# Performance work log

Hardware: AMD Instinct MI355X
Metric: run time of the kernel (lower is better)

## Reference

```python
import jax, jax.numpy as jnp
import numpy as np

N = 20000   # nodes
E = 40000   # directed edges
F_IN = 13   # dataset.num_features
G = 1000    # graphs in batch
DIMS = [(13, 32), (32, 64), (64, 64)]  # (M_in, M_out) per NNConv layer


def setup_inputs() -> dict:
    key = jax.random.key(0)
    ks = list(jax.random.split(key, 32))
    inp = {}
    inp["x"] = jax.random.normal(ks[0], (N, F_IN), jnp.float32)
    inp["edge_index"] = jax.random.randint(ks[1], (2, E), 0, N, dtype=jnp.int32)
    inp["edge_attr"] = jax.random.uniform(ks[2], (E, 5), dtype=jnp.float32)
    inp["batch"] = jnp.sort(jax.random.randint(ks[3], (N,), 0, G, dtype=jnp.int32))
    i = 4
    for l, (mi, mo) in enumerate(DIMS):
        inp[f"w1_{l}"] = jax.random.normal(ks[i], (5, 128), jnp.float32) / np.sqrt(5.0).astype(np.float32); i += 1
        inp[f"b1_{l}"] = jnp.zeros((128,), jnp.float32)
        inp[f"w2_{l}"] = jax.random.normal(ks[i], (128, mi * mo), jnp.float32) / np.sqrt(128.0).astype(np.float32); i += 1
        inp[f"b2_{l}"] = jnp.zeros((mi * mo,), jnp.float32)
        inp[f"root_{l}"] = jax.random.normal(ks[i], (mi, mo), jnp.float32) / np.sqrt(float(mi)).astype(np.float32); i += 1
        inp[f"bias_{l}"] = jnp.zeros((mo,), jnp.float32)
    inp["fc1_w"] = jax.random.normal(ks[i], (64, 32), jnp.float32) / 8.0; i += 1
    inp["fc1_b"] = jnp.zeros((32,), jnp.float32)
    inp["fc2_w"] = jax.random.normal(ks[i], (32, 16), jnp.float32) / np.sqrt(32.0).astype(np.float32); i += 1
    inp["fc2_b"] = jnp.zeros((16,), jnp.float32)
    inp["fc3_w"] = jax.random.normal(ks[i], (16, 1), jnp.float32) / 4.0; i += 1
    inp["fc3_b"] = jnp.zeros((1,), jnp.float32)
    return inp


def _nnconv(x, src, dst, edge_attr, w1, b1, w2, b2, root, bias, mi, mo):
    # edge MLP: [E,5] -> [E,128] -> [E, mi*mo] per-edge weight matrices
    h = jax.nn.relu(edge_attr @ w1 + b1)
    We = (h @ w2 + b2).reshape(-1, mi, mo)          # [E, mi, mo]
    msg = jnp.einsum('ei,eio->eo', x[src], We)      # gather + per-edge matmul
    agg = jax.ops.segment_sum(msg, dst, num_segments=x.shape[0])  # scatter-add
    return x @ root + agg + bias                    # NNConv root weight + bias


def _forward(x, edge_index, edge_attr, batch, convs, fc1_w, fc1_b, fc2_w, fc2_b, fc3_w, fc3_b):
    src, dst = edge_index[0], edge_index[1]
    for (mi, mo), (w1, b1, w2, b2, root, bias) in zip(DIMS, convs):
        x = jax.nn.elu(_nnconv(x, src, dst, edge_attr, w1, b1, w2, b2, root, bias, mi, mo))
    # scatter_mean pooling over graphs
    sums = jax.ops.segment_sum(x, batch, num_segments=G)
    cnt = jax.ops.segment_sum(jnp.ones((x.shape[0],), x.dtype), batch, num_segments=G)
    xg = sums / jnp.maximum(cnt, 1.0)[:, None]
    xg = jax.nn.elu(xg @ fc1_w + fc1_b)
    xg = jax.nn.elu(xg @ fc2_w + fc2_b)
    return (xg @ fc3_w + fc3_b).reshape(-1)


def reference(x, edge_index, edge_attr, batch,
              w1_0, b1_0, w2_0, b2_0, root_0, bias_0,
              w1_1, b1_1, w2_1, b2_1, root_1, bias_1,
              w1_2, b1_2, w2_2, b2_2, root_2, bias_2,
              fc1_w, fc1_b, fc2_w, fc2_b, fc3_w, fc3_b):
    convs = [(w1_0, b1_0, w2_0, b2_0, root_0, bias_0),
             (w1_1, b1_1, w2_1, b2_1, root_1, bias_1),
             (w1_2, b1_2, w2_2, b2_2, root_2, bias_2)]
    return _forward(x, edge_index, edge_attr, batch, convs,
                    fc1_w, fc1_b, fc2_w, fc2_b, fc3_w, fc3_b)
```

## Files before the change

### kernel.cpp

```cpp
#include <hip/hip_runtime.h>
#include <stdint.h>
#include <math.h>

typedef _Float16 half8_t __attribute__((ext_vector_type(8)));
typedef float floatx4 __attribute__((ext_vector_type(4)));

#define NN 20000
#define NE 40000
#define NG 1000
#define NBLK 313
#define NSPLIT 4

__global__ __launch_bounds__(256) void prep_fused_kernel(
    const float* __restrict__ x, _Float16* __restrict__ e16,
    const float* __restrict__ w2a, const float* __restrict__ b2a, _Float16* __restrict__ oa,
    const float* __restrict__ w2b, const float* __restrict__ b2b, _Float16* __restrict__ ob,
    const float* __restrict__ w2c, const float* __restrict__ b2c, _Float16* __restrict__ oc,
    int* __restrict__ deg)
{
  if (blockIdx.x < 1250) {
    int idx = blockIdx.x * 256 + threadIdx.x;
    int n = idx >> 4, i = idx & 15;
    e16[idx] = (i < 13) ? (_Float16)x[(size_t)n * 13 + i] : (_Float16)0.f;
    return;
  }
  if (blockIdx.x >= 1680) {
    int n = (blockIdx.x - 1680) * 256 + threadIdx.x;
    if (n < NN) deg[n] = 0;
    return;
  }
  const int TOT0 = 68 * 2 * 64, TOT1 = 132 * 4 * 64, TOT2 = 264 * 4 * 64;
  int idx = (blockIdx.x - 1250) * 256 + threadIdx.x;
  const float *w2, *b2; _Float16* op; int mi, mo, mpsh, CT;
  if (idx < TOT0) { w2 = w2a; b2 = b2a; op = oa; mi = 13; mo = 32; mpsh = 4; CT = 2; }
  else if (idx < TOT0 + TOT1) { idx -= TOT0; w2 = w2b; b2 = b2b; op = ob; mi = 32; mo = 64; mpsh = 5; CT = 4; }
  else if (idx < TOT0 + TOT1 + TOT2) { idx -= TOT0 + TOT1; w2 = w2c; b2 = b2c; op = oc; mi = 64; mo = 64; mpsh = 6; CT = 4; }
  else return;
  int l = idx & 63;
  int ct = (idx >> 6) % CT;
  int c = idx / (64 * CT);
  int q = l >> 4;
  int n = ct * 16 + (l & 15);
  int mask = (1 << mpsh) - 1;
  half8_t v;
#pragma unroll
  for (int j = 0; j < 8; ++j) {
    int r = c * 32 + q * 8 + j;
    int k = r >> mpsh, i = r & mask;
    float f = 0.f;
    if (i < mi) {
      if (k < 128) f = w2[(size_t)(k * mi + i) * mo + n];
      else if (k == 128) f = b2[(size_t)i * mo + n];
    }
    v[j] = (_Float16)f;
  }
  *(half8_t*)(op + (size_t)idx * 8) = v;
}

__global__ __launch_bounds__(256) void deg_kernel(const int* __restrict__ dst, int* __restrict__ deg) {
  int e = blockIdx.x * 256 + threadIdx.x;
  if (e < NE) atomicAdd(&deg[dst[e]], 1);
}

__global__ __launch_bounds__(1024) void scan_kernel(
    const int* __restrict__ deg, int* __restrict__ row_ptr, int* __restrict__ cursor)
{
  constexpr int CH = 20;
  __shared__ int wsum[16];
  int t = threadIdx.x;
  int lane = t & 63, w = t >> 6;
  int base = t * CH;
  int local[CH];
#pragma unroll
  for (int i = 0; i < CH; ++i) {
    int n = base + i;
    local[i] = (n < NN) ? deg[n] : 0;
  }
  int s = 0;
#pragma unroll
  for (int i = 0; i < CH; ++i) s += local[i];
  int sc = s;
#pragma unroll
  for (int d = 1; d < 64; d <<= 1) {
    int v = __shfl_up(sc, d, 64);
    if (lane >= d) sc += v;
  }
  if (lane == 63) wsum[w] = sc;
  __syncthreads();
  if (w == 0 && lane < 16) {
    int v = wsum[lane];
    int scc = v;
#pragma unroll
    for (int d = 1; d < 16; d <<= 1) {
      int u = __shfl_up(scc, d, 64);
      if (lane >= d) scc += u;
    }
    wsum[lane] = scc - v;
  }
  __syncthreads();
  int run = wsum[w] + (sc - s);
#pragma unroll
  for (int i = 0; i < CH; ++i) {
    int n = base + i;
    if (n < NN) { row_ptr[n] = run; cursor[n] = run; run += local[i]; }
    else if (n == NN) row_ptr[NN] = run;
  }
}

__global__ __launch_bounds__(256) void fill_kernel(
    const int* __restrict__ dst, int* __restrict__ cursor, int* __restrict__ eids)
{
  int e = blockIdx.x * 256 + threadIdx.x;
  if (e < NE) { int p = atomicAdd(&cursor[dst[e]], 1); eids[p] = e; }
}

template <int MIP, int MO, int NCC, int KCNT>
__global__ __launch_bounds__(256, 4) void msg9_kernel(
    const float* __restrict__ ea, const float* __restrict__ w1,
    const float* __restrict__ b1, const _Float16* __restrict__ xe,
    const int* __restrict__ src,
    const _Float16* __restrict__ w2h, _Float16* __restrict__ msgp)
{
  constexpr int EPB = 128;
  constexpr int CT = MO / 16;
  constexpr int CHB = CT * 1024;
  constexpr int XV = (MIP == 64) ? 2 : 1;
  constexpr int KH = (KCNT + 1) >> 1;

  __shared__ uint4 wsb[2][CHB / 16];
  __shared__ _Float16 h16[KCNT * EPB];
  __shared__ float w1s[5 * 128 + 128];

  const int t = threadIdx.x;
  const int wave = t >> 6, lane = t & 63;
  const int l15 = lane & 15, q = lane >> 4;
  const int split = blockIdx.x / NBLK;
  const int e0 = (blockIdx.x % NBLK) * EPB;
  const int c0 = NCC * split;
  const int kg0 = KCNT * split;

  const char* wgp = (const char*)w2h + (size_t)c0 * CHB;
  uint4 ra4, rb4; uint2 ra2, rb2;
  if constexpr (CT == 4) {
    ra4 = *(const uint4*)(wgp + t * 16);
    rb4 = *(const uint4*)(wgp + CHB + t * 16);
  } else {
    ra2 = *(const uint2*)(wgp + t * 8);
    rb2 = *(const uint2*)(wgp + CHB + t * 8);
  }

  const int wbase = wave * 32;
  half8_t xf[2][XV];
#pragma unroll
  for (int s = 0; s < 2; ++s) {
    int eg = e0 + wbase + s * 16 + l15; if (eg >= NE) eg = NE - 1;
    const _Float16* xr = xe + (size_t)src[eg] * MIP;
    int i0 = (MIP == 16) ? (q & 1) * 8 : q * 8;
    xf[s][0] = *(const half8_t*)(xr + i0);
    if constexpr (MIP == 64)
      xf[s][XV - 1] = *(const half8_t*)(xr + 32 + q * 8);
  }

  const int te = t & 127;
  float ear[5];
  {
    int eg = e0 + te; if (eg >= NE) eg = NE - 1;
#pragma unroll
    for (int j = 0; j < 5; ++j) ear[j] = ea[(size_t)eg * 5 + j];
  }
  for (int i = t; i < 768; i += 256) w1s[i] = (i < 640) ? w1[i] : b1[i - 640];
  __syncthreads();

  {
    int kh = t >> 7;
    int klo = kh * KH;
    int khi = klo + KH; if (khi > KCNT) khi = KCNT;
    for (int kl = klo; kl < khi; ++kl) {
      int kg = kg0 + kl;
      float v;
      if (kg < 128) {
        v = w1s[640 + kg];
#pragma unroll
        for (int j = 0; j < 5; ++j) v = fmaf(ear[j], w1s[j * 128 + kg], v);
        v = fmaxf(v, 0.f);
      } else v = (kg == 128) ? 1.f : 0.f;
      h16[kl * EPB + te] = (_Float16)v;
    }
  }
  __syncthreads();

  floatx4 acc[2][CT];
#pragma unroll
  for (int s = 0; s < 2; ++s)
#pragma unroll
    for (int b = 0; b < CT; ++b) acc[s][b] = (floatx4){0.f, 0.f, 0.f, 0.f};

#pragma unroll 2
  for (int cc = 0; cc < NCC; ++cc) {
    const bool odd = (cc & 1) != 0;
    if constexpr (CT == 4) wsb[cc & 1][t] = odd ? rb4 : ra4;
    else ((uint2*)wsb[cc & 1])[t] = odd ? rb2 : ra2;
    if (cc + 2 < NCC) {
      const char* np = wgp + (size_t)(cc + 2) * CHB;
      if constexpr (CT == 4) {
        if (odd) rb4 = *(const uint4*)(np + t * 16); else ra4 = *(const uint4*)(np + t * 16);
      } else {
        if (odd) rb2 = *(const uint2*)(np + t * 8); else ra2 = *(const uint2*)(np + t * 8);
      }
    }
    __syncthreads();
    const _Float16* wb = (const _Float16*)wsb[cc & 1];
    half8_t bf[CT];
#pragma unroll
    for (int b = 0; b < CT; ++b)
      bf[b] = *(const half8_t*)(wb + (b * 64 + lane) * 8);
    int kl;
    if constexpr (MIP == 64) kl = cc >> 1;
    else if constexpr (MIP == 32) kl = cc;
    else kl = 2 * cc + (q >> 1);
#pragma unroll
    for (int s = 0; s < 2; ++s) {
      _Float16 hv = h16[kl * EPB + wbase + s * 16 + l15];
      half8_t af;
      if constexpr (MIP == 64) af = xf[s][cc & 1] * hv;
      else af = xf[s][0] * hv;
#pragma unroll
      for (int b = 0; b < CT; ++b)
        acc[s][b] = __builtin_amdgcn_mfma_f32_16x16x32_f16(af, bf[b], acc[s][b], 0, 0, 0);
    }
  }

  _Float16* mp = msgp + (size_t)split * NE * MO;
#pragma unroll
  for (int s = 0; s < 2; ++s) {
    int rowb = wbase + s * 16 + q * 4;
#pragma unroll
    for (int b = 0; b < CT; ++b) {
      int n = b * 16 + l15;
#pragma unroll
      for (int r = 0; r < 4; ++r) {
        int row = rowb + r;
        int e = e0 + row;
        if (e < NE) mp[(size_t)e * MO + n] = (_Float16)acc[s][b][r];
      }
    }
  }
}

template <int MIN_, int XST, int MO, int FINAL>
__global__ __launch_bounds__(256) void gather_kernel(
    const _Float16* __restrict__ e16in, const float* __restrict__ root,
    const float* __restrict__ bias, const int* __restrict__ row_ptr,
    const int* __restrict__ eids, const _Float16* __restrict__ msgp,
    _Float16* __restrict__ oute, float* __restrict__ outf)
{
  constexpr int NPB = 256 / MO;
  int n = blockIdx.x * NPB + threadIdx.x / MO;
  int o = threadIdx.x % MO;
  if (n >= NN) return;
  float a = bias[o];
#pragma unroll
  for (int i = 0; i < MIN_; ++i)
    a = fmaf((float)e16in[(size_t)n * XST + i], root[i * MO + o], a);
  int r0 = row_ptr[n], r1 = row_ptr[n + 1];
  for (int j = r0; j < r1; ++j) {
    int e = eids[j];
#pragma unroll
    for (int s = 0; s < NSPLIT; ++s)
      a += (float)msgp[((size_t)s * NE + e) * MO + o];
  }
  if constexpr (FINAL) {
    outf[(size_t)n * MO + o] = a;
  } else {
    float v = a > 0.f ? a : (expf(a) - 1.f);
    oute[(size_t)n * MO + o] = (_Float16)v;
  }
}

__global__ __launch_bounds__(64) void pool_fc_kernel(
    const float* __restrict__ xn2, const int* __restrict__ batch,
    const float* __restrict__ f1w, const float* __restrict__ f1b,
    const float* __restrict__ f2w, const float* __restrict__ f2b,
    const float* __restrict__ f3w, const float* __restrict__ f3b,
    float* __restrict__ out)
{
  __shared__ float xg[64]; __shared__ float a1[32]; __shared__ float a2[16];
  int g = blockIdx.x, t = threadIdx.x;
  int lo = 0, hi = NN;
  while (lo < hi) { int m = (lo + hi) >> 1; if (batch[m] < g) lo = m + 1; else hi = m; }
  int start = lo; hi = NN;
  while (lo < hi) { int m = (lo + hi) >> 1; if (batch[m] <= g) lo = m + 1; else hi = m; }
  int end = lo;
  float acc = 0.f;
  for (int n = start; n < end; ++n) {
    float v = xn2[(size_t)n * 64 + t];
    acc += v > 0.f ? v : (expf(v) - 1.f);
  }
  float c = (end > start) ? (float)(end - start) : 1.f;
  xg[t] = acc / c;
  __syncthreads();
  if (t < 32) {
    float a = f1b[t];
    for (int i = 0; i < 64; ++i) a = fmaf(xg[i], f1w[i * 32 + t], a);
    a1[t] = a > 0.f ? a : (expf(a) - 1.f);
  }
  __syncthreads();
  if (t < 16) {
    float a = f2b[t];
    for (int i = 0; i < 32; ++i) a = fmaf(a1[i], f2w[i * 16 + t], a);
    a2[t] = a > 0.f ? a : (expf(a) - 1.f);
  }
  __syncthreads();
  if (t == 0) {
    float a = f3b[0];
    for (int i = 0; i < 16; ++i) a = fmaf(a2[i], f3w[i], a);
    out[g] = a;
  }
}

extern "C" void kernel_launch(void* const* d_in, const int* in_sizes, int n_in,
                              void* d_out, int out_size, void* d_ws, size_t ws_size,
                              hipStream_t stream)
{
  const float* x_in  = (const float*)d_in[0];
  const int*   ei    = (const int*)d_in[1];
  const float* ea    = (const float*)d_in[2];
  const int*   batch = (const int*)d_in[3];
  const float* W1[3] = {(const float*)d_in[4],  (const float*)d_in[10], (const float*)d_in[16]};
  const float* B1[3] = {(const float*)d_in[5],  (const float*)d_in[11], (const float*)d_in[17]};
  const float* W2[3] = {(const float*)d_in[6],  (const float*)d_in[12], (const float*)d_in[18]};
  const float* B2[3] = {(const float*)d_in[7],  (const float*)d_in[13], (const float*)d_in[19]};
  const float* RT[3] = {(const float*)d_in[8],  (const float*)d_in[14], (const float*)d_in[20]};
  const float* BS[3] = {(const float*)d_in[9],  (const float*)d_in[15], (const float*)d_in[21]};
  const float* f1w = (const float*)d_in[22]; const float* f1b = (const float*)d_in[23];
  const float* f2w = (const float*)d_in[24]; const float* f2b = (const float*)d_in[25];
  const float* f3w = (const float*)d_in[26]; const float* f3b = (const float*)d_in[27];

  char* ws = (char*)d_ws;
  size_t off = 0;
  auto alloc = [&](size_t bytes) { void* p = ws + off; off += (bytes + 255) & ~(size_t)255; return p; };
  float*    xn2   = (float*)alloc((size_t)NN * 64 * 4);
  _Float16* e16_0 = (_Float16*)alloc((size_t)NN * 16 * 2);
  _Float16* e16_1 = (_Float16*)alloc((size_t)NN * 32 * 2);
  _Float16* e16_2 = (_Float16*)alloc((size_t)NN * 64 * 2);
  _Float16* w2h0  = (_Float16*)alloc((size_t)68 * 2048);
  _Float16* w2h1  = (_Float16*)alloc((size_t)132 * 4096);
  _Float16* w2h2  = (_Float16*)alloc((size_t)264 * 4096);
  _Float16* msgp  = (_Float16*)alloc((size_t)NSPLIT * NE * 64 * 2);
  int*      deg     = (int*)alloc((size_t)NN * 4);
  int*      row_ptr = (int*)alloc((size_t)(NN + 1) * 4);
  int*      cursor  = (int*)alloc((size_t)NN * 4);
  int*      eids    = (int*)alloc((size_t)NE * 4);

  const int* srcp = ei;
  const int* dstp = ei + NE;

  prep_fused_kernel<<<1680 + (NN + 255) / 256, 256, 0, stream>>>(
      x_in, e16_0, W2[0], B2[0], w2h0, W2[1], B2[1], w2h1, W2[2], B2[2], w2h2, deg);
  deg_kernel<<<(NE + 255) / 256, 256, 0, stream>>>(dstp, deg);
  scan_kernel<<<1, 1024, 0, stream>>>(deg, row_ptr, cursor);
  fill_kernel<<<(NE + 255) / 256, 256, 0, stream>>>(dstp, cursor, eids);

  msg9_kernel<16, 32, 17, 34><<<NBLK * NSPLIT, 256, 0, stream>>>(
      ea, W1[0], B1[0], e16_0, srcp, w2h0, msgp);
  gather_kernel<13, 16, 32, 0><<<(NN + 7) / 8, 256, 0, stream>>>(
      e16_0, RT[0], BS[0], row_ptr, eids, msgp, e16_1, xn2);

  msg9_kernel<32, 64, 33, 33><<<NBLK * NSPLIT, 256, 0, stream>>>(
      ea, W1[1], B1[1], e16_1, srcp, w2h1, msgp);
  gather_kernel<32, 32, 64, 0><<<(NN + 3) / 4, 256, 0, stream>>>(
      e16_1, RT[1], BS[1], row_ptr, eids, msgp, e16_2, xn2);

  msg9_kernel<64, 64, 66, 33><<<NBLK * NSPLIT, 256, 0, stream>>>(
      ea, W1[2], B1[2], e16_2, srcp, w2h2, msgp);
  gather_kernel<64, 64, 64, 1><<<(NN + 3) / 4, 256, 0, stream>>>(
      e16_2, RT[2], BS[2], row_ptr, eids, msgp, e16_2, xn2);

  pool_fc_kernel<<<NG, 64, 0, stream>>>(xn2, batch, f1w, f1b, f2w, f2b, f3w, f3b, (float*)d_out);
}
```

Before: 291.8 us.

## Add msgN kernel with per-wave output columns and 128-edge tiles for layers 2-3

Adds a new message kernel for the 64-wide output layers. Each wave owns 16 output columns and loops over 8 edge row-tiles held in registers, so each loaded weight fragment is reused across 128 edges instead of being reloaded per small edge tile. Hidden activations are computed once into LDS as fp16 and scaled into the x fragments before each MFMA. The cost is higher register pressure from 8 accumulators and the x fragments, which the kernel caps by requesting 3 blocks per CU in its launch bounds.

```diff
diff --git a/kernel.cpp b/kernel.cpp
--- a/kernel.cpp
+++ b/kernel.cpp
@@ -243,6 +243,127 @@
         int e = e0 + row;
         if (e < NE) mp[(size_t)e * MO + n] = (_Float16)acc[s][b][r];
       }
+    }
+  }
+}
+
+template <int MIP, int NCC, int KCNT>
+__global__ __launch_bounds__(256, 3) void msgN_kernel(
+    const float* __restrict__ ea, const float* __restrict__ w1,
+    const float* __restrict__ b1, const _Float16* __restrict__ xe,
+    const int* __restrict__ src,
+    const _Float16* __restrict__ w2h, _Float16* __restrict__ msgp)
+{
+  constexpr int EPB = 128;
+  constexpr int MO = 64;
+  constexpr int CT = 4;
+  constexpr int CHB = CT * 1024;
+  constexpr int XV = (MIP == 64) ? 2 : 1;
+  constexpr int KH = (KCNT + 1) >> 1;
+  constexpr int NG8 = KCNT / 8;
+  constexpr int JT = KCNT % 8;
+  constexpr int NGT = (KCNT + 7) / 8;
+
+  __shared__ _Float16 h16[NGT * EPB * 8];
+  __shared__ float w1s[5 * 128 + 128];
+
+  const int t = threadIdx.x;
+  const int wave = t >> 6, lane = t & 63;
+  const int l15 = lane & 15, q = lane >> 4;
+  const int split = blockIdx.x / NBLK;
+  const int e0 = (blockIdx.x % NBLK) * EPB;
+  const int c0 = NCC * split;
+  const int kg0 = KCNT * split;
+  const char* wgp = (const char*)w2h + (size_t)c0 * CHB;
+
+  const int te = t & 127;
+  float ear[5];
+  {
+    int eg = e0 + te; if (eg >= NE) eg = NE - 1;
+#pragma unroll
+    for (int j = 0; j < 5; ++j) ear[j] = ea[(size_t)eg * 5 + j];
+  }
+  for (int i = t; i < 768; i += 256) w1s[i] = (i < 640) ? w1[i] : b1[i - 640];
+  __syncthreads();
+
+  {
+    int kh = t >> 7;
+    int klo = kh * KH;
+    int khi = klo + KH; if (khi > KCNT) khi = KCNT;
+    for (int kl = klo; kl < khi; ++kl) {
+      int kg = kg0 + kl;
+      float v;
+      if (kg < 128) {
+        v = w1s[640 + kg];
+#pragma unroll
+        for (int j = 0; j < 5; ++j) v = fmaf(ear[j], w1s[j * 128 + kg], v);
+        v = fmaxf(v, 0.f);
+      } else v = (kg == 128) ? 1.f : 0.f;
+      h16[((kl >> 3) * EPB + te) * 8 + (kl & 7)] = (_Float16)v;
+    }
+  }
+  __syncthreads();
+
+  half8_t xf[8][XV];
+#pragma unroll
+  for (int m = 0; m < 8; ++m) {
+    int eg = e0 + m * 16 + l15; if (eg >= NE) eg = NE - 1;
+    const _Float16* xr = xe + (size_t)src[eg] * MIP;
+    xf[m][0] = *(const half8_t*)(xr + q * 8);
+    if constexpr (MIP == 64)
+      xf[m][XV - 1] = *(const half8_t*)(xr + 32 + q * 8);
+  }
+
+  floatx4 acc[8];
+#pragma unroll
+  for (int m = 0; m < 8; ++m) acc[m] = (floatx4){0.f, 0.f, 0.f, 0.f};
+
+  const char* wq = wgp + (size_t)wave * 1024 + (size_t)lane * 16;
+
+#pragma unroll
+  for (int g = 0; g < NGT; ++g) {
+    half8_t h8[8];
+#pragma unroll
+    for (int m = 0; m < 8; ++m)
+      h8[m] = *(const half8_t*)(h16 + ((size_t)g * EPB + m * 16 + l15) * 8);
+    const int jn = (g < NG8) ? 8 : JT;
+#pragma unroll
+    for (int j = 0; j < 8; ++j) {
+      if (j < jn) {
+        const int kl = g * 8 + j;
+        if constexpr (MIP == 64) {
+#pragma unroll
+          for (int hf = 0; hf < 2; ++hf) {
+            const int cc = kl * 2 + hf;
+            half8_t bf = *(const half8_t*)(wq + (size_t)cc * CHB);
+#pragma unroll
+            for (int m = 0; m < 8; ++m) {
+              half8_t af = xf[m][hf] * h8[m][j];
+              acc[m] = __builtin_amdgcn_mfma_f32_16x16x32_f16(af, bf, acc[m], 0, 0, 0);
+            }
+          }
+        } else {
+          const int cc = kl;
+          half8_t bf = *(const half8_t*)(wq + (size_t)cc * CHB);
+#pragma unroll
+          for (int m = 0; m < 8; ++m) {
+            half8_t af = xf[m][0] * h8[m][j];
+            acc[m] = __builtin_amdgcn_mfma_f32_16x16x32_f16(af, bf, acc[m], 0, 0, 0);
+          }
+        }
+      }
+    }
+  }
+
+  _Float16* mp = msgp + (size_t)split * NE * MO;
+  const int n = wave * 16 + l15;
+#pragma unroll
+  for (int m = 0; m < 8; ++m) {
+    int rowb = m * 16 + q * 4;
+#pragma unroll
+    for (int r = 0; r < 4; ++r) {
+      int e = e0 + rowb + r;
+      if (e < NE) mp[(size_t)e * MO + n] = (_Float16)acc[m][r];
     }
   }
 }
@@ -366,12 +487,12 @@
   gather_kernel<13, 16, 32, 0><<<(NN + 7) / 8, 256, 0, stream>>>(
       e16_0, RT[0], BS[0], row_ptr, eids, msgp, e16_1, xn2);
 
-  msg9_kernel<32, 64, 33, 33><<<NBLK * NSPLIT, 256, 0, stream>>>(
+  msgN_kernel<32, 33, 33><<<NBLK * NSPLIT, 256, 0, stream>>>(
       ea, W1[1], B1[1], e16_1, srcp, w2h1, msgp);
   gather_kernel<32, 32, 64, 0><<<(NN + 3) / 4, 256, 0, stream>>>(
       e16_1, RT[1], BS[1], row_ptr, eids, msgp, e16_2, xn2);
 
-  msg9_kernel<64, 64, 66, 33><<<NBLK * NSPLIT, 256, 0, stream>>>(
+  msgN_kernel<64, 66, 33><<<NBLK * NSPLIT, 256, 0, stream>>>(
       ea, W1[2], B1[2], e16_2, srcp, w2h2, msgp);
   gather_kernel<64, 64, 64, 1><<<(NN + 3) / 4, 256, 0, stream>>>(
       e16_2, RT[2], BS[2], row_ptr, eids, msgp, e16_2, xn2);
```

New measurement: 306.9 us. 1.05x slower.
